# Kernel optimization log

Hardware: AMD Instinct MI355X
Metric: run time of the kernel (lower is better)

The kernel has to match this reference:

```python
import jax, jax.numpy as jnp
import numpy as np

N, IN_DIM, HID, TASK, L = 8192, 128, 128, 64, 2
NEG_SLOPE = 0.01
MASK_VAL = -9e15


def setup_inputs() -> dict:
    key = jax.random.key(0)
    ks = jax.random.split(key, 20)
    s_in = 1.0 / np.sqrt(IN_DIM)
    s_h = 1.0 / np.sqrt(HID)
    s_g = 1.0 / np.sqrt(HID + TASK)
    return {
        "h": jax.random.normal(ks[0], (N, IN_DIM), jnp.float32),
        "adj": jax.random.randint(ks[1], (N, N), 0, 2, jnp.int32),
        "z": jax.random.normal(ks[2], (N, TASK), jnp.float32),
        "Wp": jax.random.normal(ks[3], (IN_DIM, HID), jnp.float32) * s_in,
        "bp": jnp.zeros((HID,), jnp.float32),
        "Wm": jax.random.normal(ks[4], (L, HID, HID), jnp.float32) * s_h,
        "bm": jnp.zeros((L, HID), jnp.float32),
        "Wg": jax.random.normal(ks[5], (L, HID + TASK, HID), jnp.float32) * s_g,
        "bg": jnp.zeros((L, HID), jnp.float32),
        "Wk": jax.random.normal(ks[6], (L, HID, HID), jnp.float32) * s_h,
        "bk": jnp.zeros((L, HID), jnp.float32),
        "Wq": jax.random.normal(ks[7], (L, HID, HID), jnp.float32) * s_h,
        "bq": jnp.zeros((L, HID), jnp.float32),
        "a1": jax.random.normal(ks[8], (L, HID), jnp.float32) * s_h,
        "a2": jax.random.normal(ks[9], (L, HID), jnp.float32) * s_h,
    }


def reference(h, adj, z, Wp, bp, Wm, bm, Wg, bg, Wk, bk, Wq, bq, a1, a2):
    # initial projection
    h = h @ Wp + bp  # [N, HID]
    mask = adj > 0   # [N, N]
    total_loss = jnp.float32(0.0)
    n_layers = Wm.shape[0]
    for l in range(n_layers):
        raw = jax.nn.relu(h @ Wm[l] + bm[l])                              # [N, HID]
        gate = jax.nn.sigmoid(jnp.concatenate([h, z], axis=1) @ Wg[l] + bg[l])
        gm = gate * raw                                                   # gated message
        total_loss = total_loss + jnp.sum(jnp.abs(gate)) / gate.size
        q = gm @ Wq[l] + bq[l]                                            # [N, HID]
        k = h @ Wk[l] + bk[l]                                             # [N, HID]
        # e[i, j] = leaky_relu(k[j]. a1 + q[i]. a2) -- equivalent to the
        # original repeat/cat then (attn_input @ a)
        e = jax.nn.leaky_relu((k @ a1[l])[None, :] + (q @ a2[l])[:, None],
                              negative_slope=NEG_SLOPE)                   # [N, N]
        e = jnp.where(mask, e, jnp.float32(MASK_VAL))
        attn = jax.nn.softmax(e, axis=1)                                  # softmax over j
        agg = attn.T @ gm                                                 # [N, HID]
        h = (agg + h) * 0.5
    return h, total_loss / n_layers
```

## Files before the change

kernel.cpp:

```cpp
#include <hip/hip_runtime.h>
#include <hip/hip_bf16.h>
#include <hip/hip_fp16.h>

#define NN 8192
#define HIDD 128
#define NLAY 2

typedef __attribute__((ext_vector_type(8))) short bf16x8;
typedef __attribute__((ext_vector_type(4))) float f32x4;

static __device__ __forceinline__ unsigned short f2b(float x) {
    __hip_bfloat16 h = __float2bfloat16(x);
    return *reinterpret_cast<unsigned short*>(&h);
}
static __device__ __forceinline__ unsigned short f2h(float x) {
    __half h = __float2half(x);
    return *reinterpret_cast<unsigned short*>(&h);
}
static __device__ __forceinline__ float h2f(unsigned short u) {
    __half h = *reinterpret_cast<__half*>(&u);
    return __half2float(h);
}

static __device__ __forceinline__ unsigned long long spread4(unsigned long long x) {
    x = (x | (x << 24)) & 0x000000ff000000ffULL;
    x = (x | (x << 12)) & 0x000f000f000f000fULL;
    x = (x | (x << 6))  & 0x0303030303030303ULL;
    x = (x | (x << 3))  & 0x1111111111111111ULL;
    return x;
}

__global__ void k_pre(const int* __restrict__ adj, unsigned long long* __restrict__ bm,
                      const float* __restrict__ hin, const float* __restrict__ Wp,
                      const float* __restrict__ bp, float* __restrict__ hout,
                      const float* __restrict__ Wk, const float* __restrict__ Wq,
                      const float* __restrict__ a1, const float* __restrict__ a2,
                      const float* __restrict__ bk, const float* __restrict__ bq,
                      float* __restrict__ wka, float* __restrict__ wqa,
                      float* __restrict__ scal, float* __restrict__ lossacc) {
    __shared__ float ht[16][128];
    int b = blockIdx.x;
    int tid = threadIdx.x;
    if (b < 512) {
        int i0 = b * 16;
#pragma unroll
        for (int r = 0; r < 2; r++) {
            int q = r * 256 + tid;
            ((float4*)ht)[q] = ((const float4*)(hin + (size_t)i0 * 128))[q];
        }
        __syncthreads();
        int c = tid & 127, half = tid >> 7;
        float acc[8];
        float b0 = bp[c];
#pragma unroll
        for (int m = 0; m < 8; m++) acc[m] = b0;
        for (int k = 0; k < 128; k += 4) {
            float w0 = Wp[k * 128 + c], w1 = Wp[(k + 1) * 128 + c];
            float w2 = Wp[(k + 2) * 128 + c], w3 = Wp[(k + 3) * 128 + c];
#pragma unroll
            for (int m = 0; m < 8; m++) {
                float4 hv = *(const float4*)&ht[half + 2 * m][k];
                acc[m] = fmaf(hv.x, w0, acc[m]);
                acc[m] = fmaf(hv.y, w1, acc[m]);
                acc[m] = fmaf(hv.z, w2, acc[m]);
                acc[m] = fmaf(hv.w, w3, acc[m]);
            }
        }
#pragma unroll
        for (int m = 0; m < 8; m++) hout[(size_t)(i0 + half + 2 * m) * 128 + c] = acc[m];
    } else if (b < 514) {
        int l = b - 512;
        const float* a1L = a1 + l * 128;
        const float* a2L = a2 + l * 128;
        if (tid < 128) {
            const float* W1 = Wk + (size_t)l * 16384 + (size_t)tid * 128;
            const float* W2 = Wq + (size_t)l * 16384 + (size_t)tid * 128;
            float s1 = 0.f, s2 = 0.f;
            for (int c = 0; c < 128; c++) {
                s1 = fmaf(W1[c], a1L[c], s1);
                s2 = fmaf(W2[c], a2L[c], s2);
            }
            wka[l * 128 + tid] = s1;
            wqa[l * 128 + tid] = s2;
        } else if (tid == 128) {
            float s = 0.f;
            for (int c = 0; c < 128; c++) s = fmaf(bk[l * 128 + c], a1L[c], s);
            scal[l * 2 + 0] = s;
        } else if (tid == 129) {
            float s = 0.f;
            for (int c = 0; c < 128; c++) s = fmaf(bq[l * 128 + c], a2L[c], s);
            scal[l * 2 + 1] = s;
        } else if (tid == 130 && l == 0) {
            lossacc[0] = 0.f;
        }
    } else {
        const long totalg = (long)NN * (NN / 256);
        int lane = tid & 63, w = tid >> 6;
        long nb = (long)gridDim.x - 514;
        long g = (long)(b - 514) * 4 + w;
        long ng = nb * 4;
        for (; g < totalg; g += ng) {
            int4 v = ((const int4*)adj)[g * 64 + lane];
            unsigned long long B0 = __ballot(v.x > 0);
            unsigned long long B1 = __ballot(v.y > 0);
            unsigned long long B2 = __ballot(v.z > 0);
            unsigned long long B3 = __ballot(v.w > 0);
            if (lane < 4) {
                int sh = lane * 16;
                unsigned long long W = spread4((B0 >> sh) & 0xFFFF)
                                     | (spread4((B1 >> sh) & 0xFFFF) << 1)
                                     | (spread4((B2 >> sh) & 0xFFFF) << 2)
                                     | (spread4((B3 >> sh) & 0xFFFF) << 3);
                bm[g * 4 + lane] = W;
            }
        }
    }
}

__global__ void k_btrans(const unsigned* __restrict__ bm32, unsigned* __restrict__ bt32) {
    __shared__ unsigned t[64][65];
    int bi = blockIdx.x >> 2;
    int bj = blockIdx.x & 3;
    int i0 = bi * 64, jw0 = bj * 64;
    int tid = threadIdx.x;
    int c = tid & 63, r4 = tid >> 6;
#pragma unroll
    for (int rr = 0; rr < 16; rr++) {
        int ir = rr * 4 + r4;
        t[ir][c] = bm32[(size_t)(i0 + ir) * 256 + jw0 + c];
    }
    __syncthreads();
#pragma unroll
    for (int rr = 0; rr < 16; rr++) {
        int jr = rr * 4 + r4;
        bt32[(size_t)(jw0 + jr) * NN + i0 + c] = t[c][jr];
    }
}

__global__ void k_gm(const float* __restrict__ hbase, const unsigned short* __restrict__ aggs16,
                     int nslab, float* __restrict__ hstore, const float* __restrict__ z,
                     const float* __restrict__ Wm, const float* __restrict__ bmv,
                     const float* __restrict__ Wg, const float* __restrict__ bgv,
                     const float* __restrict__ wka, const float* __restrict__ wqa,
                     const float* __restrict__ scal,
                     unsigned short* __restrict__ gmT, float* __restrict__ ek,
                     float* __restrict__ ek01, float* __restrict__ eq_,
                     float* __restrict__ eq01_, float* __restrict__ S,
                     float* __restrict__ lossacc) {
    __shared__ float ht[8][128];
    __shared__ float zt[8][64];
    __shared__ unsigned short tb[128][16];
    __shared__ float redk[4][4], redq[4][4], redl[4];
    int i0 = blockIdx.x * 8;
    int tid = threadIdx.x;
    {
        int q = tid;
        float4 hv = ((const float4*)(hbase + (size_t)i0 * 128))[q];
        if (nslab > 0) {
            float sx = 0.f, sy = 0.f, sz = 0.f, sw = 0.f;
            for (int s = 0; s < nslab; s++) {
                ushort4 a = ((const ushort4*)(aggs16 + (size_t)s * NN * HIDD))[(size_t)i0 * 32 + q];
                sx += h2f(a.x); sy += h2f(a.y); sz += h2f(a.z); sw += h2f(a.w);
            }
            hv.x = (hv.x + sx) * 0.5f;
            hv.y = (hv.y + sy) * 0.5f;
            hv.z = (hv.z + sz) * 0.5f;
            hv.w = (hv.w + sw) * 0.5f;
            ((float4*)(hstore + (size_t)i0 * 128))[q] = hv;
        }
        ((float4*)ht)[q] = hv;
    }
    if (tid < 128) ((float4*)zt)[tid] = ((const float4*)(z + (size_t)i0 * 64))[tid];
    __syncthreads();
    int c = tid & 127, half = tid >> 7;
    float am[4], ag[4];
    float bm0 = bmv[c], bg0 = bgv[c];
#pragma unroll
    for (int m = 0; m < 4; m++) { am[m] = bm0; ag[m] = bg0; }
    for (int k = 0; k < 128; k += 4) {
        float wm0 = Wm[k * 128 + c], wm1 = Wm[(k + 1) * 128 + c];
        float wm2 = Wm[(k + 2) * 128 + c], wm3 = Wm[(k + 3) * 128 + c];
        float wg0 = Wg[k * 128 + c], wg1 = Wg[(k + 1) * 128 + c];
        float wg2 = Wg[(k + 2) * 128 + c], wg3 = Wg[(k + 3) * 128 + c];
#pragma unroll
        for (int m = 0; m < 4; m++) {
            float4 hv = *(const float4*)&ht[half + 2 * m][k];
            am[m] = fmaf(hv.x, wm0, am[m]);
            am[m] = fmaf(hv.y, wm1, am[m]);
            am[m] = fmaf(hv.z, wm2, am[m]);
            am[m] = fmaf(hv.w, wm3, am[m]);
            ag[m] = fmaf(hv.x, wg0, ag[m]);
            ag[m] = fmaf(hv.y, wg1, ag[m]);
            ag[m] = fmaf(hv.z, wg2, ag[m]);
            ag[m] = fmaf(hv.w, wg3, ag[m]);
        }
    }
    for (int k = 0; k < 64; k += 4) {
        float wg0 = Wg[(128 + k) * 128 + c], wg1 = Wg[(129 + k) * 128 + c];
        float wg2 = Wg[(130 + k) * 128 + c], wg3 = Wg[(131 + k) * 128 + c];
#pragma unroll
        for (int m = 0; m < 4; m++) {
            float4 zv = *(const float4*)&zt[half + 2 * m][k];
            ag[m] = fmaf(zv.x, wg0, ag[m]);
            ag[m] = fmaf(zv.y, wg1, ag[m]);
            ag[m] = fmaf(zv.z, wg2, ag[m]);
            ag[m] = fmaf(zv.w, wg3, ag[m]);
        }
    }
    float lsum = 0.f;
    float gmv[4];
#pragma unroll
    for (int m = 0; m < 4; m++) {
        float gate = 1.f / (1.f + __expf(-ag[m]));
        lsum += gate;
        gmv[m] = gate * fmaxf(am[m], 0.f);
        tb[c][half + 2 * m] = f2b(gmv[m]);
    }
    float wkac = wka[c], wqac = wqa[c];
    int wid = tid >> 6, lane = tid & 63;
#pragma unroll
    for (int m = 0; m < 4; m++) {
        float vk = ht[half + 2 * m][c] * wkac;
        float vq = gmv[m] * wqac;
#pragma unroll
        for (int o = 32; o; o >>= 1) {
            vk += __shfl_down(vk, o);
            vq += __shfl_down(vq, o);
        }
        if (lane == 0) { redk[wid][m] = vk; redq[wid][m] = vq; }
    }
#pragma unroll
    for (int o = 32; o; o >>= 1) lsum += __shfl_down(lsum, o);
    if (lane == 0) redl[wid] = lsum;
    __syncthreads();
    if (tid < 8) {
        int r = tid, hf = r & 1, m = r >> 1;
        const float LOG2E = 1.4426950408889634f;
        float kdl = (redk[2 * hf][m] + redk[2 * hf + 1][m] + scal[0]) * LOG2E;
        float ql = (redq[2 * hf][m] + redq[2 * hf + 1][m] + scal[1]) * LOG2E;
        ek[i0 + r] = exp2f(kdl);
        ek01[i0 + r] = exp2f(0.01f * kdl);
        eq_[i0 + r] = exp2f(ql);
        eq01_[i0 + r] = exp2f(0.01f * ql);
        S[i0 + r] = 0.f;
    }
    if (tid == 0) atomicAdd(lossacc, redl[0] + redl[1] + redl[2] + redl[3]);
    if (tid < 128) *(int4*)&gmT[(size_t)tid * NN + i0] = *(int4*)&tb[tid][0];
}

__global__ void k_stats(const unsigned* __restrict__ bm32, const float* __restrict__ ek,
                        const float* __restrict__ ek01, const float* __restrict__ eq_,
                        const float* __restrict__ eq01_, float* __restrict__ S) {
    __shared__ float2 ep[2048];
    int bid = blockIdx.x;
    int rs = bid >> 2, ch = bid & 3;
    int r0 = rs * 16;
    int base = ch * 2048;
    int tid = threadIdx.x, lane = tid & 63, w = tid >> 6;
#pragma unroll
    for (int p = 0; p < 2; p++) {
        int idx = p * 1024 + tid * 4;
        float4 a = *(const float4*)(ek + base + idx);
        float4 b = *(const float4*)(ek01 + base + idx);
        ep[idx + 0] = make_float2(a.x, b.x);
        ep[idx + 1] = make_float2(a.y, b.y);
        ep[idx + 2] = make_float2(a.z, b.z);
        ep[idx + 3] = make_float2(a.w, b.w);
    }
    float eqv[4], eq01v[4];
    unsigned mrow[4];
#pragma unroll
    for (int t = 0; t < 4; t++) {
        int row = r0 + w * 4 + t;
        eqv[t] = eq_[row];
        eq01v[t] = eq01_[row];
        mrow[t] = bm32[(size_t)row * 256 + ch * 64 + lane];
    }
    float s[4] = {0.f, 0.f, 0.f, 0.f};
    __syncthreads();
#pragma unroll 4
    for (int jj = 0; jj < 32; jj++) {
        float2 e = ep[jj * 64 + lane];
        int widx = jj * 2 + (lane >> 5);
        int bit = lane & 31;
#pragma unroll
        for (int t = 0; t < 4; t++) {
            unsigned word = __shfl(mrow[t], widx);
            float v = fmaxf(e.x * eqv[t], e.y * eq01v[t]);
            s[t] += ((word >> bit) & 1) ? v : 0.f;
        }
    }
#pragma unroll
    for (int t = 0; t < 4; t++) {
        float v = s[t];
#pragma unroll
        for (int o = 32; o; o >>= 1) v += __shfl_xor(v, o);
        if (lane == 0) atomicAdd(&S[r0 + w * 4 + t], v);
    }
}

#define BJ 128
#define KC 64
#define NSPLIT 16
#define NCH ((NN / NSPLIT) / KC)

__launch_bounds__(256, 3)
__global__ void k_attn_gemm(const unsigned* __restrict__ bt32, const float* __restrict__ ek,
                            const float* __restrict__ ek01, const float* __restrict__ eq_,
                            const float* __restrict__ eq01_, const float* __restrict__ S,
                            const unsigned short* __restrict__ gmT,
                            float* __restrict__ aggf, unsigned short* __restrict__ part16,
                            int use_atomic) {
    int id = blockIdx.x;
    int sp = id & 15;
    int jb = id >> 4;
    int j0 = jb * BJ;
    int ibase = sp * (NN / NSPLIT);
    int tid = threadIdx.x;
    int lane = tid & 63;
    int w = tid >> 6;
    int lo = lane & 15;
    int qw = lane >> 4;

    __shared__ __align__(16) unsigned short G_l[2][HIDD * KC];
    __shared__ __align__(16) unsigned mask_l[2][4 * KC];
    __shared__ __align__(16) float e_l[2][KC];
    __shared__ __align__(16) float e01_l[2][KC];

    float ekA   = ek  [j0 + w * 32 + lo];
    float ekA01 = ek01[j0 + w * 32 + lo];
    float ekB   = ek  [j0 + w * 32 + lo + 16];
    float ekB01 = ek01[j0 + w * 32 + lo + 16];

    int jq0 = j0 >> 5;
    int4 greg[4];
    unsigned mreg;
    float ereg, e01reg, sreg;

    {
        int ig = ibase;
#pragma unroll
        for (int r = 0; r < 4; r++) {
            int slot = r * 256 + tid;
            int hh = slot >> 3, sd = slot & 7;
            greg[r] = *(const int4*)(gmT + (size_t)hh * NN + ig + sd * 8);
        }
        mreg = bt32[(size_t)(jq0 + w) * NN + ig + lane];
        ereg = eq_[ig + lane];
        e01reg = eq01_[ig + lane];
        sreg = S[ig + lane];
#pragma unroll
        for (int r = 0; r < 4; r++) {
            int slot = r * 256 + tid;
            int hh = slot >> 3, sd = slot & 7;
            *(int4*)&G_l[0][hh * KC + ((sd ^ (hh & 7)) * 8)] = greg[r];
        }
        mask_l[0][tid] = mreg;
        float inv = (sreg > 0.f) ? 1.0f / sreg : 0.f;
        if (tid < KC) { e_l[0][tid] = ereg * inv; e01_l[0][tid] = e01reg * inv; }
    }
    __syncthreads();

    f32x4 acc[2][8];
#pragma unroll
    for (int a = 0; a < 2; a++)
#pragma unroll
        for (int b = 0; b < 8; b++) acc[a][b] = (f32x4){0.f, 0.f, 0.f, 0.f};

    int cur = 0;
    for (int c = 0; c < NCH; c++) {
        if (c + 1 < NCH) {
            int ig = ibase + (c + 1) * KC;
#pragma unroll
            for (int r = 0; r < 4; r++) {
                int slot = r * 256 + tid;
                int hh = slot >> 3, sd = slot & 7;
                greg[r] = *(const int4*)(gmT + (size_t)hh * NN + ig + sd * 8);
            }
            mreg = bt32[(size_t)(jq0 + w) * NN + ig + lane];
            ereg = eq_[ig + lane];
            e01reg = eq01_[ig + lane];
            sreg = S[ig + lane];
        }
#pragma unroll
        for (int kk = 0; kk < 2; kk++) {
            int kb = kk * 32 + qw * 8;
            float4 ea = *(const float4*)&e_l[cur][kb];
            float4 eb = *(const float4*)&e_l[cur][kb + 4];
            float4 fa = *(const float4*)&e01_l[cur][kb];
            float4 fb = *(const float4*)&e01_l[cur][kb + 4];
            uint4 ma = *(const uint4*)&mask_l[cur][w * 64 + kb];
            uint4 mb = *(const uint4*)&mask_l[cur][w * 64 + kb + 4];
            float ev[8] = {ea.x, ea.y, ea.z, ea.w, eb.x, eb.y, eb.z, eb.w};
            float fv[8] = {fa.x, fa.y, fa.z, fa.w, fb.x, fb.y, fb.z, fb.w};
            unsigned mw[8] = {ma.x, ma.y, ma.z, ma.w, mb.x, mb.y, mb.z, mb.w};
            union { unsigned u[4]; bf16x8 v; } A0, A1;
#pragma unroll
            for (int p = 0; p < 4; p++) {
                int e0 = 2 * p, e1 = 2 * p + 1;
                float w00 = ((mw[e0] >> lo) & 1)        ? fmaxf(ekA * ev[e0], ekA01 * fv[e0]) : 0.f;
                float w10 = ((mw[e0] >> (lo + 16)) & 1) ? fmaxf(ekB * ev[e0], ekB01 * fv[e0]) : 0.f;
                float w01 = ((mw[e1] >> lo) & 1)        ? fmaxf(ekA * ev[e1], ekA01 * fv[e1]) : 0.f;
                float w11 = ((mw[e1] >> (lo + 16)) & 1) ? fmaxf(ekB * ev[e1], ekB01 * fv[e1]) : 0.f;
                A0.u[p] = (unsigned)f2b(w00) | ((unsigned)f2b(w01) << 16);
                A1.u[p] = (unsigned)f2b(w10) | ((unsigned)f2b(w11) << 16);
            }
            __builtin_amdgcn_s_setprio(1);
#pragma unroll
            for (int hf = 0; hf < 8; hf++) {
                int hr = hf * 16 + lo;
                bf16x8 bv = *(const bf16x8*)&G_l[cur][hr * KC + ((kk * 32 + qw * 8) ^ ((hr & 7) << 3))];
                acc[0][hf] = __builtin_amdgcn_mfma_f32_16x16x32_bf16(A0.v, bv, acc[0][hf], 0, 0, 0);
                acc[1][hf] = __builtin_amdgcn_mfma_f32_16x16x32_bf16(A1.v, bv, acc[1][hf], 0, 0, 0);
            }
            __builtin_amdgcn_s_setprio(0);
        }
        if (c + 1 < NCH) {
            int nxt = cur ^ 1;
#pragma unroll
            for (int r = 0; r < 4; r++) {
                int slot = r * 256 + tid;
                int hh = slot >> 3, sd = slot & 7;
                *(int4*)&G_l[nxt][hh * KC + ((sd ^ (hh & 7)) * 8)] = greg[r];
            }
            mask_l[nxt][tid] = mreg;
            float inv = (sreg > 0.f) ? 1.0f / sreg : 0.f;
            if (tid < KC) { e_l[nxt][tid] = ereg * inv; e01_l[nxt][tid] = e01reg * inv; }
        }
        __syncthreads();
        cur ^= 1;
    }
    int row_base = w * 32 + (lane >> 4) * 4;
    int col = lane & 15;
    size_t slab = (size_t)sp * NN * HIDD;
#pragma unroll
    for (int jf = 0; jf < 2; jf++)
#pragma unroll
        for (int hf = 0; hf < 8; hf++)
#pragma unroll
            for (int r = 0; r < 4; r++) {
                int j = j0 + row_base + jf * 16 + r;
                int hcol = hf * 16 + col;
                size_t off = (size_t)j * HIDD + hcol;
                if (use_atomic) atomicAdd(&aggf[off], acc[jf][hf][r]);
                else part16[slab + off] = f2h(acc[jf][hf][r]);
            }
}

__global__ void k_combine(const unsigned short* __restrict__ acc16, const float* __restrict__ accf,
                          int nslab, int use_atomic,
                          const float* __restrict__ hin, float* __restrict__ hout,
                          const float* __restrict__ lossacc, float* __restrict__ lossout) {
    size_t i = (size_t)blockIdx.x * blockDim.x + threadIdx.x;
    float4 hv = ((const float4*)hin)[i];
    float sx = 0.f, sy = 0.f, sz = 0.f, sw = 0.f;
    if (use_atomic) {
        float4 a = ((const float4*)accf)[i];
        sx = a.x; sy = a.y; sz = a.z; sw = a.w;
    } else {
        for (int s = 0; s < nslab; s++) {
            ushort4 a = ((const ushort4*)(acc16 + (size_t)s * NN * HIDD))[i];
            sx += h2f(a.x); sy += h2f(a.y); sz += h2f(a.z); sw += h2f(a.w);
        }
    }
    float4 o;
    o.x = (sx + hv.x) * 0.5f;
    o.y = (sy + hv.y) * 0.5f;
    o.z = (sz + hv.z) * 0.5f;
    o.w = (sw + hv.w) * 0.5f;
    ((float4*)hout)[i] = o;
    if (lossout != nullptr && i == 0)
        lossout[0] = lossacc[0] * (1.0f / (float)((size_t)NN * HIDD * NLAY));
}

extern "C" void kernel_launch(void* const* d_in, const int* in_sizes, int n_in,
                              void* d_out, int out_size, void* d_ws, size_t ws_size,
                              hipStream_t stream) {
    const float* h_in = (const float*)d_in[0];
    const int* adj = (const int*)d_in[1];
    const float* z = (const float*)d_in[2];
    const float* Wp = (const float*)d_in[3];
    const float* bp = (const float*)d_in[4];
    const float* Wm = (const float*)d_in[5];
    const float* bmv = (const float*)d_in[6];
    const float* Wg = (const float*)d_in[7];
    const float* bgv = (const float*)d_in[8];
    const float* Wk = (const float*)d_in[9];
    const float* bk = (const float*)d_in[10];
    const float* Wq = (const float*)d_in[11];
    const float* bq = (const float*)d_in[12];
    const float* a1 = (const float*)d_in[13];
    const float* a2 = (const float*)d_in[14];
    float* out = (float*)d_out;

    char* ws = (char*)d_ws;
    unsigned long long* BM64 = (unsigned long long*)(ws + 0);
    unsigned* BM32 = (unsigned*)(ws + 0);
    unsigned* BT32 = (unsigned*)(ws + (8ull << 20));
    float* hcur = (float*)(ws + (16ull << 20));
    unsigned short* gmT = (unsigned short*)(ws + (20ull << 20));
    float* ek    = (float*)(ws + (22ull << 20));
    float* ek01  = (float*)(ws + (22ull << 20) + (32ull << 10));
    float* eq    = (float*)(ws + (22ull << 20) + (64ull << 10));
    float* eq01  = (float*)(ws + (22ull << 20) + (96ull << 10));
    float* S     = (float*)(ws + (22ull << 20) + (128ull << 10));
    float* wka   = (float*)(ws + (22ull << 20) + (160ull << 10));
    float* wqa   = (float*)(ws + (22ull << 20) + (164ull << 10));
    float* scal  = (float*)(ws + (22ull << 20) + (168ull << 10));
    float* lossacc = (float*)(ws + (22ull << 20) + (172ull << 10));
    float* agg = (float*)(ws + (23ull << 20));
    unsigned short* part16 = (unsigned short*)(ws + (27ull << 20));
    int use_atomic = (ws_size < (60ull << 20)) ? 1 : 0;
    int nslab = use_atomic ? 1 : NSPLIT;

    k_pre<<<2048, 256, 0, stream>>>(adj, BM64, h_in, Wp, bp, hcur,
                                    Wk, Wq, a1, a2, bk, bq, wka, wqa, scal, lossacc);
    k_btrans<<<512, 256, 0, stream>>>(BM32, BT32);

    for (int l = 0; l < NLAY; l++) {
        k_gm<<<NN / 8, 256, 0, stream>>>(
            hcur, part16, (l > 0 && !use_atomic) ? nslab : 0, hcur,
            z, Wm + (size_t)l * 128 * 128, bmv + l * 128,
            Wg + (size_t)l * 192 * 128, bgv + l * 128,
            wka + l * 128, wqa + l * 128, scal + l * 2,
            gmT, ek, ek01, eq, eq01, S, lossacc);
        k_stats<<<(NN / 16) * 4, 256, 0, stream>>>(BM32, ek, ek01, eq, eq01, S);
        if (use_atomic) hipMemsetAsync(agg, 0, (size_t)NN * HIDD * 4, stream);
        k_attn_gemm<<<(NN / BJ) * NSPLIT, 256, 0, stream>>>(BT32, ek, ek01, eq, eq01, S, gmT,
                                                            agg, part16, use_atomic);
        if (use_atomic && l == 0) {
            k_combine<<<NN * HIDD / 4 / 256, 256, 0, stream>>>(
                part16, agg, 1, 1, hcur, hcur, lossacc, (float*)nullptr);
        }
    }
    k_combine<<<NN * HIDD / 4 / 256, 256, 0, stream>>>(
        part16, agg, nslab, use_atomic, hcur, out, lossacc, out + (size_t)NN * HIDD);
}
```

Baseline: 271.4 us.

## Stage gm tiles via direct global-to-LDS loads and vectorize attention weight construction

Replaces the register-staged global loads and LDS stores of the gmT tile with global_load_lds direct-to-LDS transfers, pre-swizzling the source address so the existing XOR layout is kept. This removes the register round trip and the separate ds_write pass. The attention weight construction now uses packed float2 math, a packed bf16 convert instruction, and branchless sign-extended mask selection in place of per-element conditionals. The risk is synchronization correctness, since the async LDS writes rely on the existing barrier at the end of each iteration.

Result: faster. 254.5 us (-6.2%).

```diff
diff --git a/kernel.cpp b/kernel.cpp
--- a/kernel.cpp
+++ b/kernel.cpp
@@ -8,6 +8,9 @@
 
 typedef __attribute__((ext_vector_type(8))) short bf16x8;
 typedef __attribute__((ext_vector_type(4))) float f32x4;
+typedef __attribute__((ext_vector_type(2))) float v2f;
+typedef const void __attribute__((address_space(1)))* gas_ptr;
+typedef void __attribute__((address_space(3)))* las_ptr;
 
 static __device__ __forceinline__ unsigned short f2b(float x) {
     __hip_bfloat16 h = __float2bfloat16(x);
@@ -321,6 +324,8 @@
     int w = tid >> 6;
     int lo = lane & 15;
     int qw = lane >> 4;
+    int shA = 31 - lo;
+    int shB = 15 - lo;
 
     __shared__ __align__(16) unsigned short G_l[2][HIDD * KC];
     __shared__ __align__(16) unsigned mask_l[2][4 * KC];
@@ -331,30 +336,33 @@
     float ekA01 = ek01[j0 + w * 32 + lo];
     float ekB   = ek  [j0 + w * 32 + lo + 16];
     float ekB01 = ek01[j0 + w * 32 + lo + 16];
+    v2f ekA2   = {ekA, ekA},     ekA012 = {ekA01, ekA01};
+    v2f ekB2   = {ekB, ekB},     ekB012 = {ekB01, ekB01};
 
     int jq0 = j0 >> 5;
-    int4 greg[4];
     unsigned mreg;
     float ereg, e01reg, sreg;
+    int wbase = (tid & 192) * 8;
+
+#define STAGE_G(buf, igx)                                                                   \
+    {                                                                                       \
+        _Pragma("unroll")                                                                   \
+        for (int r = 0; r < 4; r++) {                                                       \
+            int slot = r * 256 + tid;                                                       \
+            int hh = slot >> 3, sd = slot & 7;                                              \
+            const unsigned short* gsrc = gmT + (size_t)hh * NN + (igx) + ((sd ^ (hh & 7)) * 8); \
+            __builtin_amdgcn_global_load_lds((gas_ptr)gsrc,                                 \
+                (las_ptr)&G_l[buf][r * 2048 + wbase], 16, 0, 0);                            \
+        }                                                                                   \
+    }
 
     {
         int ig = ibase;
-#pragma unroll
-        for (int r = 0; r < 4; r++) {
-            int slot = r * 256 + tid;
-            int hh = slot >> 3, sd = slot & 7;
-            greg[r] = *(const int4*)(gmT + (size_t)hh * NN + ig + sd * 8);
-        }
+        STAGE_G(0, ig);
         mreg = bt32[(size_t)(jq0 + w) * NN + ig + lane];
         ereg = eq_[ig + lane];
         e01reg = eq01_[ig + lane];
         sreg = S[ig + lane];
-#pragma unroll
-        for (int r = 0; r < 4; r++) {
-            int slot = r * 256 + tid;
-            int hh = slot >> 3, sd = slot & 7;
-            *(int4*)&G_l[0][hh * KC + ((sd ^ (hh & 7)) * 8)] = greg[r];
-        }
         mask_l[0][tid] = mreg;
         float inv = (sreg > 0.f) ? 1.0f / sreg : 0.f;
         if (tid < KC) { e_l[0][tid] = ereg * inv; e01_l[0][tid] = e01reg * inv; }
@@ -371,12 +379,7 @@
     for (int c = 0; c < NCH; c++) {
         if (c + 1 < NCH) {
             int ig = ibase + (c + 1) * KC;
-#pragma unroll
-            for (int r = 0; r < 4; r++) {
-                int slot = r * 256 + tid;
-                int hh = slot >> 3, sd = slot & 7;
-                greg[r] = *(const int4*)(gmT + (size_t)hh * NN + ig + sd * 8);
-            }
+            STAGE_G(cur ^ 1, ig);
             mreg = bt32[(size_t)(jq0 + w) * NN + ig + lane];
             ereg = eq_[ig + lane];
             e01reg = eq01_[ig + lane];
@@ -385,25 +388,26 @@
 #pragma unroll
         for (int kk = 0; kk < 2; kk++) {
             int kb = kk * 32 + qw * 8;
-            float4 ea = *(const float4*)&e_l[cur][kb];
-            float4 eb = *(const float4*)&e_l[cur][kb + 4];
-            float4 fa = *(const float4*)&e01_l[cur][kb];
-            float4 fb = *(const float4*)&e01_l[cur][kb + 4];
             uint4 ma = *(const uint4*)&mask_l[cur][w * 64 + kb];
             uint4 mb = *(const uint4*)&mask_l[cur][w * 64 + kb + 4];
-            float ev[8] = {ea.x, ea.y, ea.z, ea.w, eb.x, eb.y, eb.z, eb.w};
-            float fv[8] = {fa.x, fa.y, fa.z, fa.w, fb.x, fb.y, fb.z, fb.w};
             unsigned mw[8] = {ma.x, ma.y, ma.z, ma.w, mb.x, mb.y, mb.z, mb.w};
             union { unsigned u[4]; bf16x8 v; } A0, A1;
 #pragma unroll
             for (int p = 0; p < 4; p++) {
-                int e0 = 2 * p, e1 = 2 * p + 1;
-                float w00 = ((mw[e0] >> lo) & 1)        ? fmaxf(ekA * ev[e0], ekA01 * fv[e0]) : 0.f;
-                float w10 = ((mw[e0] >> (lo + 16)) & 1) ? fmaxf(ekB * ev[e0], ekB01 * fv[e0]) : 0.f;
-                float w01 = ((mw[e1] >> lo) & 1)        ? fmaxf(ekA * ev[e1], ekA01 * fv[e1]) : 0.f;
-                float w11 = ((mw[e1] >> (lo + 16)) & 1) ? fmaxf(ekB * ev[e1], ekB01 * fv[e1]) : 0.f;
-                A0.u[p] = (unsigned)f2b(w00) | ((unsigned)f2b(w01) << 16);
-                A1.u[p] = (unsigned)f2b(w10) | ((unsigned)f2b(w11) << 16);
+                v2f e2 = *(const v2f*)&e_l[cur][kb + 2 * p];
+                v2f f2 = *(const v2f*)&e01_l[cur][kb + 2 * p];
+                v2f tA = __builtin_elementwise_max(ekA2 * e2, ekA012 * f2);
+                v2f tB = __builtin_elementwise_max(ekB2 * e2, ekB012 * f2);
+                unsigned wA, wB;
+                asm("v_cvt_pk_bf16_f32 %0, %1, %2" : "=v"(wA) : "v"(tA.x), "v"(tA.y));
+                asm("v_cvt_pk_bf16_f32 %0, %1, %2" : "=v"(wB) : "v"(tB.x), "v"(tB.y));
+                unsigned m0 = mw[2 * p], m1 = mw[2 * p + 1];
+                unsigned a0 = (unsigned)(((int)(m0 << shA)) >> 31);
+                unsigned a1 = (unsigned)(((int)(m1 << shA)) >> 31);
+                unsigned b0 = (unsigned)(((int)(m0 << shB)) >> 31);
+                unsigned b1 = (unsigned)(((int)(m1 << shB)) >> 31);
+                A0.u[p] = wA & ((a0 & 0xFFFFu) | (a1 & 0xFFFF0000u));
+                A1.u[p] = wB & ((b0 & 0xFFFFu) | (b1 & 0xFFFF0000u));
             }
             __builtin_amdgcn_s_setprio(1);
 #pragma unroll
@@ -417,12 +421,6 @@
         }
         if (c + 1 < NCH) {
             int nxt = cur ^ 1;
-#pragma unroll
-            for (int r = 0; r < 4; r++) {
-                int slot = r * 256 + tid;
-                int hh = slot >> 3, sd = slot & 7;
-                *(int4*)&G_l[nxt][hh * KC + ((sd ^ (hh & 7)) * 8)] = greg[r];
-            }
             mask_l[nxt][tid] = mreg;
             float inv = (sreg > 0.f) ? 1.0f / sreg : 0.f;
             if (tid < KC) { e_l[nxt][tid] = ereg * inv; e01_l[nxt][tid] = e01reg * inv; }
@@ -445,6 +443,7 @@
                 if (use_atomic) atomicAdd(&aggf[off], acc[jf][hf][r]);
                 else part16[slab + off] = f2h(acc[jf][hf][r]);
             }
+#undef STAGE_G
 }
 
 __global__ void k_combine(const unsigned short* __restrict__ acc16, const float* __restrict__ accf,
```
